# Kernel optimization log

Hardware: AMD Instinct MI355X
Metric: run time of the kernel (lower is better)

Reference implementation:

```python
import jax, jax.numpy as jnp
import numpy as np

BN_EPS = 1e-5
C = 128  # channels (hardcoded by feed_forward convs)


def _bn(v, gamma, beta, mean, var):
    # BatchNorm1d in inference form over channel axis of [B, C, N]
    scale = gamma / jnp.sqrt(var + BN_EPS)
    return (v - mean[:, None]) * scale[:, None] + beta[:, None]


def setup_inputs() -> dict:
    key = jax.random.key(0)
    ks = jax.random.split(key, 8)
    B, N = 8, 2048
    s = 0.05
    return {
        "x": jax.random.normal(ks[0], (B, N, C), jnp.float32),
        "Wq": jax.random.normal(ks[1], (C // 4, C), jnp.float32) * s,
        "Wk": jax.random.normal(ks[2], (C // 4, C), jnp.float32) * s,
        "Wv": jax.random.normal(ks[3], (C, C), jnp.float32) * s,
        "bv": jnp.zeros((C,), jnp.float32),
        "Wt": jax.random.normal(ks[4], (C, C), jnp.float32) * s,
        "bt": jnp.zeros((C,), jnp.float32),
        "g1": jnp.ones((C,), jnp.float32),
        "b1": jnp.zeros((C,), jnp.float32),
        "m1": jnp.zeros((C,), jnp.float32),
        "v1": jnp.ones((C,), jnp.float32),
        "W1": jax.random.normal(ks[5], (512, C), jnp.float32) * s,
        "bf1": jnp.zeros((512,), jnp.float32),
        "W2": jax.random.normal(ks[6], (C, 512), jnp.float32) * s,
        "bf2": jnp.zeros((C,), jnp.float32),
        "g2": jnp.ones((C,), jnp.float32),
        "b2": jnp.zeros((C,), jnp.float32),
        "m2": jnp.zeros((C,), jnp.float32),
        "v2": jnp.ones((C,), jnp.float32),
    }


def reference(x, Wq, Wk, Wv, bv, Wt, bt, g1, b1, m1, v1,
              W1, bf1, W2, bf2, g2, b2, m2, v2):
    # x: [B, N, C] -> work in [B, C, N] layout like the torch module
    xc = jnp.transpose(x, (0, 2, 1))                      # [B, C, N]
    # q_conv(x).permute -> [B, N, C/4]; k_conv -> [B, C/4, N]
    x_q = jnp.einsum('bnc,oc->bno', x, Wq)                # [B, N, C/4]
    x_k = jnp.einsum('bnc,oc->bon', x, Wk)                # [B, C/4, N]
    x_v = jnp.einsum('bnc,oc->bon', x, Wv) + bv[:, None]  # [B, C, N]

    energy = jnp.einsum('bnd,bdm->bnm', x_q, x_k)         # [B, N, N]
    scale = jnp.sqrt(jnp.asarray(C, x.dtype))             # sqrt(x_v.shape[-2])
    attention = jax.nn.softmax(energy / scale, axis=-1)   # [B, N, N]
    x_r = jnp.einsum('bcn,bnm->bcm', x_v, attention)      # [B, C, N]

    t = jnp.einsum('oc,bcn->bon', Wt, xc - x_r) + bt[:, None]
    x_r2 = jax.nn.relu(_bn(t, g1, b1, m1, v1))
    h = xc + x_r2                                         # [B, C, N]

    residual = h
    f = jax.nn.relu(jnp.einsum('oc,bcn->bon', W1, h) + bf1[:, None])
    f = jnp.einsum('of,bfn->bon', W2, f) + bf2[:, None]
    out = _bn(residual + f, g2, b2, m2, v2)               # [B, C, N]
    return jnp.transpose(out, (0, 2, 1))                  # [B, N, C]
```

## Files before the change

kernel.cpp:

```cpp
#include <hip/hip_runtime.h>
#include <hip/hip_bf16.h>

#define BDIM 256
#define NPTS (8 * 2048)
#define CC 128
#define DD 32
#define FF 512
#define NN 2048
#define SCALE 0.08838834764831845f

typedef float f32x4 __attribute__((ext_vector_type(4)));
typedef short s16x8 __attribute__((ext_vector_type(8)));
typedef unsigned short ushort_t;

__device__ __forceinline__ ushort_t bf16r(float x) {
    __hip_bfloat16 h = __float2bfloat16(x);
    return *reinterpret_cast<ushort_t*>(&h);
}
__device__ __forceinline__ float bf16tof(ushort_t u) {
    unsigned v = ((unsigned)u) << 16;
    return *reinterpret_cast<float*>(&v);
}
__device__ __forceinline__ unsigned pack2(float a, float b) {
    return ((unsigned)bf16r(b) << 16) | (unsigned)bf16r(a);
}

__global__ void k_cvt_all(const float* __restrict__ W1, const float* __restrict__ W2,
                          const float* __restrict__ Wq, const float* __restrict__ Wk,
                          const float* __restrict__ Wv, const float* __restrict__ Wt,
                          ushort_t* __restrict__ dst) {
    int i = blockIdx.x * BDIM + threadIdx.x;
    const float* src; int off;
    if (i < 16384)      { src = W1; off = 0; }
    else if (i < 32768) { src = W2; off = 16384; }
    else if (i < 33792) { src = Wq; off = 32768; }
    else if (i < 34816) { src = Wk; off = 33792; }
    else if (i < 38912) { src = Wv; off = 34816; }
    else                { src = Wt; off = 38912; }
    float4 v = ((const float4*)src)[i - off];
    *(uint2*)(dst + (long)i * 4) = make_uint2(pack2(v.x, v.y), pack2(v.z, v.w));
}

__global__ __launch_bounds__(256) void k_proj(
        const float* __restrict__ x, const ushort_t* __restrict__ Wb,
        const float* __restrict__ bv,
        ushort_t* __restrict__ qg, ushort_t* __restrict__ kg,
        ushort_t* __restrict__ vTg) {
    __shared__ ushort_t xs[32][136];
    __shared__ ushort_t qks[32][72];
    __shared__ ushort_t vs[32][136];
    long base = (long)blockIdx.x * 32;
    int b = (int)(base >> 11);
    int n0 = (int)(base & (NN - 1));
    int t = threadIdx.x, w = t >> 6, l = t & 63, a = l & 15, g = l >> 4;
    {
        const float4* xg4 = (const float4*)(x + base * CC);
        #pragma unroll
        for (int rep = 0; rep < 4; ++rep) {
            int i = rep * BDIM + t;
            float4 v4 = xg4[i];
            int p = i >> 5, c4 = (i & 31) * 4;
            *(uint2*)&xs[p][c4] = make_uint2(pack2(v4.x, v4.y), pack2(v4.z, v4.w));
        }
    }
    s16x8 bF[3][4];
    #pragma unroll
    for (int ct = 0; ct < 3; ++ct) {
        int ctg = w * 3 + ct;
        #pragma unroll
        for (int ki = 0; ki < 4; ++ki)
            bF[ct][ki] = *(const s16x8*)(Wb + ((long)(ctg * 16 + a)) * CC + ki * 32 + g * 8);
    }
    __syncthreads();
    #pragma unroll
    for (int rt = 0; rt < 2; ++rt) {
        s16x8 aF[4];
        #pragma unroll
        for (int ki = 0; ki < 4; ++ki)
            aF[ki] = *(const s16x8*)&xs[rt * 16 + a][ki * 32 + g * 8];
        #pragma unroll
        for (int ct = 0; ct < 3; ++ct) {
            f32x4 acc = (f32x4){0.f, 0.f, 0.f, 0.f};
            #pragma unroll
            for (int ki = 0; ki < 4; ++ki)
                acc = __builtin_amdgcn_mfma_f32_16x16x32_bf16(aF[ki], bF[ct][ki], acc, 0, 0, 0);
            int ctg = w * 3 + ct;
            int oc = ctg * 16 + a;
            float bias = (oc >= 64) ? bv[oc - 64] : 0.f;
            #pragma unroll
            for (int r = 0; r < 4; ++r) {
                int p = rt * 16 + g * 4 + r;
                float val = acc[r] + bias;
                if (oc < 64) qks[p][oc] = bf16r(val);
                else         vs[p][oc - 64] = bf16r(val);
            }
        }
    }
    __syncthreads();
    {
        int p = t >> 3, c = (t & 7) * 4;
        *(uint2*)(qg + (base + p) * DD + c) = *(const uint2*)&qks[p][c];
        *(uint2*)(kg + (base + p) * DD + c) = *(const uint2*)&qks[p][32 + c];
    }
    #pragma unroll
    for (int rep = 0; rep < 2; ++rep) {
        int i = rep * BDIM + t;
        int c = i & 127, nch = i >> 7;
        int p0 = nch * 8;
        uint4 r;
        r.x = (unsigned)vs[p0+0][c] | ((unsigned)vs[p0+1][c] << 16);
        r.y = (unsigned)vs[p0+2][c] | ((unsigned)vs[p0+3][c] << 16);
        r.z = (unsigned)vs[p0+4][c] | ((unsigned)vs[p0+5][c] << 16);
        r.w = (unsigned)vs[p0+6][c] | ((unsigned)vs[p0+7][c] << 16);
        *(uint4*)(vTg + ((long)(b * CC + c)) * NN + n0 + p0) = r;
    }
}

__global__ __launch_bounds__(256) void k_rowstats(
        const ushort_t* __restrict__ qg, const ushort_t* __restrict__ kg,
        float* __restrict__ rowinv) {
    __shared__ float ps[4][64];
    int b = blockIdx.x >> 5;
    int nt = (blockIdx.x & 31) * 64;
    int t = threadIdx.x, w = t >> 6, l = t & 63, a = l & 15, g = l >> 4;
    s16x8 qA[4];
    #pragma unroll
    for (int s = 0; s < 4; ++s)
        qA[s] = *(const s16x8*)(qg + ((long)(b * NN + nt + s*16 + a)) * DD + g*8);
    float sm[16];
    #pragma unroll
    for (int i = 0; i < 16; ++i) sm[i] = 0.f;
    s16x8 kB = *(const s16x8*)(kg + ((long)(b * NN + w * 16 + a)) * DD + g*8);
    for (int it = 0; it < 32; ++it) {
        s16x8 kBn;
        if (it < 31)
            kBn = *(const s16x8*)(kg + ((long)(b * NN + ((it+1)*4 + w)*16 + a)) * DD + g*8);
        #pragma unroll
        for (int s = 0; s < 4; ++s) {
            f32x4 D = (f32x4){0.f, 0.f, 0.f, 0.f};
            D = __builtin_amdgcn_mfma_f32_16x16x32_bf16(qA[s], kB, D, 0, 0, 0);
            #pragma unroll
            for (int r = 0; r < 4; ++r)
                sm[s * 4 + r] += __expf(D[r] * SCALE);
        }
        kB = kBn;
    }
    #pragma unroll
    for (int off = 1; off < 16; off <<= 1)
        #pragma unroll
        for (int ix = 0; ix < 16; ++ix)
            sm[ix] += __shfl_xor(sm[ix], off, 64);
    if (a == 0) {
        #pragma unroll
        for (int s = 0; s < 4; ++s)
            #pragma unroll
            for (int r = 0; r < 4; ++r)
                ps[w][s * 16 + g * 4 + r] = sm[s * 4 + r];
    }
    __syncthreads();
    if (t < 64) {
        float S = ps[0][t] + ps[1][t] + ps[2][t] + ps[3][t];
        rowinv[(long)b * NN + nt + t] = 1.f / S;
    }
}

__global__ __launch_bounds__(512) void k_pv(
        const ushort_t* __restrict__ qg, const ushort_t* __restrict__ kg,
        const ushort_t* __restrict__ vTg, const float* __restrict__ rowinv,
        const float* __restrict__ x, const ushort_t* __restrict__ Wtb,
        const float* __restrict__ bt,
        const float* __restrict__ g1, const float* __restrict__ b1,
        const float* __restrict__ m1, const float* __restrict__ v1,
        ushort_t* __restrict__ hb) {
    __shared__ ushort_t qs[2][64][40];
    __shared__ ushort_t ks[32][40];
    __shared__ ushort_t vTs[2][128][72];
    __shared__ ushort_t pT[32][72];
    __shared__ float rin_s[2][64];
    __shared__ ushort_t xb[32][136];
    __shared__ ushort_t ds[32][136];
    int b = blockIdx.x >> 6;
    int m0 = (blockIdx.x & 63) * 32;
    int t = threadIdx.x, w = t >> 6, l = t & 63, a = l & 15, g = l >> 4;
    int nsub = w & 3, msub = w >> 2;
    const ushort_t* vTb = vTg + (long)b * CC * NN;
    if (t < 128) {
        int r = t >> 2, o = (t & 3) * 8;
        *(s16x8*)&ks[r][o] = *(const s16x8*)(kg + ((long)(b * NN + m0 + r)) * DD + o);
    }
    int qr = t >> 2, qo = (t & 3) * 8;
    int c0 = t >> 3, vo0 = (t & 7) * 8;
    int c1 = (512 + t) >> 3, vo1 = (t & 7) * 8;
    uint4 qreg = make_uint4(0, 0, 0, 0), vreg0, vreg1;
    float rinreg = 0.f;
    if (t < 256) qreg = *(const uint4*)(qg + ((long)(b * NN + qr)) * DD + qo);
    vreg0 = *(const uint4*)(vTb + (long)c0 * NN + vo0);
    vreg1 = *(const uint4*)(vTb + (long)c1 * NN + vo1);
    if (t < 64) rinreg = rowinv[(long)b * NN + t];
    if (t < 256) *(uint4*)&qs[0][qr][qo] = qreg;
    *(uint4*)&vTs[0][c0][vo0] = vreg0;
    *(uint4*)&vTs[0][c1][vo1] = vreg1;
    if (t < 64) rin_s[0][t] = rinreg;

    f32x4 acc[2];
    acc[0] = (f32x4){0.f, 0.f, 0.f, 0.f};
    acc[1] = (f32x4){0.f, 0.f, 0.f, 0.f};
    int cur = 0;
    for (int it = 0; it < 32; ++it) {
        __syncthreads();
        int ntn = (it + 1) * 64;
        if (it < 31) {
            if (t < 256) qreg = *(const uint4*)(qg + ((long)(b * NN + ntn + qr)) * DD + qo);
            vreg0 = *(const uint4*)(vTb + (long)c0 * NN + ntn + vo0);
            vreg1 = *(const uint4*)(vTb + (long)c1 * NN + ntn + vo1);
            if (t < 64) rinreg = rowinv[(long)b * NN + ntn + t];
        }
        s16x8 qf = *(const s16x8*)&qs[cur][nsub * 16 + a][g * 8];
        s16x8 kf = *(const s16x8*)&ks[msub * 16 + a][g * 8];
        f32x4 e = (f32x4){0.f, 0.f, 0.f, 0.f};
        e = __builtin_amdgcn_mfma_f32_16x16x32_bf16(qf, kf, e, 0, 0, 0);
        float p[4];
        #pragma unroll
        for (int r = 0; r < 4; ++r)
            p[r] = __expf(e[r] * SCALE) * rin_s[cur][nsub * 16 + g * 4 + r];
        *(uint2*)&pT[msub * 16 + a][nsub * 16 + g * 4] =
            make_uint2(pack2(p[0], p[1]), pack2(p[2], p[3]));
        __syncthreads();
        #pragma unroll
        for (int k2 = 0; k2 < 2; ++k2) {
            s16x8 A0 = *(const s16x8*)&pT[a][k2 * 32 + g * 8];
            s16x8 A1 = *(const s16x8*)&pT[16 + a][k2 * 32 + g * 8];
            s16x8 Bf = *(const s16x8*)&vTs[cur][w * 16 + a][k2 * 32 + g * 8];
            acc[0] = __builtin_amdgcn_mfma_f32_16x16x32_bf16(A0, Bf, acc[0], 0, 0, 0);
            acc[1] = __builtin_amdgcn_mfma_f32_16x16x32_bf16(A1, Bf, acc[1], 0, 0, 0);
        }
        if (it < 31) {
            if (t < 256) *(uint4*)&qs[cur ^ 1][qr][qo] = qreg;
            *(uint4*)&vTs[cur ^ 1][c0][vo0] = vreg0;
            *(uint4*)&vTs[cur ^ 1][c1][vo1] = vreg1;
            if (t < 64) rin_s[cur ^ 1][t] = rinreg;
        }
        cur ^= 1;
    }
    long pbase = (long)b * NN + m0;
    {
        const float4* xg4 = (const float4*)(x + pbase * CC);
        #pragma unroll
        for (int rep = 0; rep < 2; ++rep) {
            int i = rep * 512 + t;
            float4 xv = xg4[i];
            int p = i >> 5, c4 = (i & 31) * 4;
            *(uint2*)&xb[p][c4] = make_uint2(pack2(xv.x, xv.y), pack2(xv.z, xv.w));
        }
    }
    __syncthreads();
    #pragma unroll
    for (int ms = 0; ms < 2; ++ms)
        #pragma unroll
        for (int r = 0; r < 4; ++r) {
            int ml = ms * 16 + g * 4 + r;
            int c = w * 16 + a;
            ds[ml][c] = bf16r(bf16tof(xb[ml][c]) - acc[ms][r]);
        }
    __syncthreads();
    {
        int ph = w & 1, fh = w >> 1;
        s16x8 aF[4];
        #pragma unroll
        for (int ki = 0; ki < 4; ++ki)
            aF[ki] = *(const s16x8*)&ds[ph * 16 + a][ki * 32 + g * 8];
        #pragma unroll
        for (int oi = 0; oi < 2; ++oi) {
            int ot = fh * 2 + oi;
            f32x4 ac = (f32x4){0.f, 0.f, 0.f, 0.f};
            #pragma unroll
            for (int ki = 0; ki < 4; ++ki) {
                s16x8 bF = *(const s16x8*)(Wtb + ((long)(ot * 16 + a)) * CC + ki * 32 + g * 8);
                ac = __builtin_amdgcn_mfma_f32_16x16x32_bf16(aF[ki], bF, ac, 0, 0, 0);
            }
            int o = ot * 16 + a;
            float sc = g1[o] * rsqrtf(v1[o] + 1e-5f);
            float mm = m1[o], bb = b1[o], bo = bt[o];
            #pragma unroll
            for (int r = 0; r < 4; ++r) {
                int p = ph * 16 + g * 4 + r;
                float tv = ((ac[r] + bo) - mm) * sc + bb;
                tv = fmaxf(tv, 0.f);
                hb[(pbase + p) * CC + o] = bf16r(bf16tof(xb[p][o]) + tv);
            }
        }
    }
}

__global__ __launch_bounds__(256) void k_ff(
        const ushort_t* __restrict__ hb, const ushort_t* __restrict__ W1b,
        const ushort_t* __restrict__ W2b,
        const float* __restrict__ bf1, const float* __restrict__ bf2,
        const float* __restrict__ g2, const float* __restrict__ b2,
        const float* __restrict__ m2, const float* __restrict__ v2,
        float* __restrict__ out) {
    __shared__ ushort_t hs[32][136];
    __shared__ ushort_t w1s[2][64][128];
    __shared__ ushort_t w2s[2][128][64];
    __shared__ ushort_t fss[32][72];
    long pbase = (long)blockIdx.x * 32;
    int t = threadIdx.x;
    int l = t & 63, wid = t >> 6;
    int ph = wid & 1, fh = wid >> 1;
    int lr = l & 15, lg = l >> 4;
    for (int i = t; i < 512; i += BDIM) {
        int r = i >> 4, c0 = (i & 15) * 8;
        *(uint4*)&hs[r][c0] = *(const uint4*)(hb + (pbase + r) * CC + c0);
    }
    #pragma unroll
    for (int rep = 0; rep < 4; ++rep) {
        int i = rep * BDIM + t;
        int r = i >> 4, c0 = (i & 15) * 8;
        *(uint4*)&w1s[0][r][c0 ^ ((r & 7) * 8)] = *(const uint4*)(W1b + (long)r * CC + c0);
    }
    #pragma unroll
    for (int rep = 0; rep < 4; ++rep) {
        int i = rep * BDIM + t;
        int r = i >> 3, c0 = (i & 7) * 8;
        *(uint4*)&w2s[0][r][c0 ^ ((r & 7) * 8)] = *(const uint4*)(W2b + (long)r * FF + c0);
    }
    __syncthreads();
    s16x8 hA[4];
    #pragma unroll
    for (int ki = 0; ki < 4; ++ki)
        hA[ki] = *(const s16x8*)&hs[ph * 16 + lr][ki * 32 + lg * 8];
    f32x4 acc2[4];
    #pragma unroll
    for (int i = 0; i < 4; ++i) acc2[i] = (f32x4){0.f, 0.f, 0.f, 0.f};

    int cur = 0;
    uint4 wrg0, wrg1, wrg2, wrg3, wrg4, wrg5, wrg6, wrg7;
    for (int fc = 0; fc < 8; ++fc) {
        if (fc) __syncthreads();
        int f0 = fc * 64;
        if (fc < 7) {
            int f0n = f0 + 64;
            int r1 = t >> 4, c1 = (t & 15) * 8;
            int r2 = t >> 3, c2 = (t & 7) * 8;
            wrg0 = *(const uint4*)(W1b + (long)(f0n + r1) * CC + c1);
            wrg1 = *(const uint4*)(W1b + (long)(f0n + 16 + r1) * CC + c1);
            wrg2 = *(const uint4*)(W1b + (long)(f0n + 32 + r1) * CC + c1);
            wrg3 = *(const uint4*)(W1b + (long)(f0n + 48 + r1) * CC + c1);
            wrg4 = *(const uint4*)(W2b + (long)r2 * FF + f0n + c2);
            wrg5 = *(const uint4*)(W2b + (long)(32 + r2) * FF + f0n + c2);
            wrg6 = *(const uint4*)(W2b + (long)(64 + r2) * FF + f0n + c2);
            wrg7 = *(const uint4*)(W2b + (long)(96 + r2) * FF + f0n + c2);
        }
        #pragma unroll
        for (int fi = 0; fi < 2; ++fi) {
            int ft = fh * 2 + fi;
            int row = ft * 16 + lr;
            f32x4 a1 = (f32x4){0.f, 0.f, 0.f, 0.f};
            #pragma unroll
            for (int ki = 0; ki < 4; ++ki) {
                int col = ki * 32 + lg * 8;
                s16x8 bfr = *(const s16x8*)&w1s[cur][row][col ^ ((row & 7) * 8)];
                a1 = __builtin_amdgcn_mfma_f32_16x16x32_bf16(hA[ki], bfr, a1, 0, 0, 0);
            }
            float bias = bf1[f0 + ft * 16 + lr];
            #pragma unroll
            for (int r = 0; r < 4; ++r) {
                float vv = fmaxf(a1[r] + bias, 0.f);
                fss[ph * 16 + lg * 4 + r][ft * 16 + lr] = bf16r(vv);
            }
        }
        __syncthreads();
        #pragma unroll
        for (int k2 = 0; k2 < 2; ++k2) {
            s16x8 afr = *(const s16x8*)&fss[ph * 16 + lr][k2 * 32 + lg * 8];
            #pragma unroll
            for (int oi = 0; oi < 4; ++oi) {
                int ot = fh * 4 + oi;
                int row = ot * 16 + lr;
                int col = k2 * 32 + lg * 8;
                s16x8 bfr = *(const s16x8*)&w2s[cur][row][col ^ ((row & 7) * 8)];
                acc2[oi] = __builtin_amdgcn_mfma_f32_16x16x32_bf16(afr, bfr, acc2[oi], 0, 0, 0);
            }
        }
        if (fc < 7) {
            int nb = cur ^ 1;
            int r1 = t >> 4, c1 = (t & 15) * 8;
            int r2 = t >> 3, c2 = (t & 7) * 8;
            *(uint4*)&w1s[nb][r1][c1 ^ ((r1 & 7) * 8)] = wrg0;
            *(uint4*)&w1s[nb][16 + r1][c1 ^ ((r1 & 7) * 8)] = wrg1;
            *(uint4*)&w1s[nb][32 + r1][c1 ^ ((r1 & 7) * 8)] = wrg2;
            *(uint4*)&w1s[nb][48 + r1][c1 ^ ((r1 & 7) * 8)] = wrg3;
            *(uint4*)&w2s[nb][r2][c2 ^ ((r2 & 7) * 8)] = wrg4;
            *(uint4*)&w2s[nb][32 + r2][c2 ^ (((32 + r2) & 7) * 8)] = wrg5;
            *(uint4*)&w2s[nb][64 + r2][c2 ^ (((64 + r2) & 7) * 8)] = wrg6;
            *(uint4*)&w2s[nb][96 + r2][c2 ^ (((96 + r2) & 7) * 8)] = wrg7;
            cur = nb;
        }
    }
    #pragma unroll
    for (int oi = 0; oi < 4; ++oi) {
        int o = (fh * 4 + oi) * 16 + lr;
        float sc = g2[o] * rsqrtf(v2[o] + 1e-5f);
        float mm = m2[o], bb = b2[o], bias2 = bf2[o];
        #pragma unroll
        for (int r = 0; r < 4; ++r) {
            int p = ph * 16 + lg * 4 + r;
            float val = bf16tof(hs[p][o]) + acc2[oi][r] + bias2;
            out[(pbase + p) * CC + o] = (val - mm) * sc + bb;
        }
    }
}

extern "C" void kernel_launch(void* const* d_in, const int* in_sizes, int n_in,
                              void* d_out, int out_size, void* d_ws, size_t ws_size,
                              hipStream_t stream) {
    const float* x   = (const float*)d_in[0];
    const float* Wq  = (const float*)d_in[1];
    const float* Wk  = (const float*)d_in[2];
    const float* Wv  = (const float*)d_in[3];
    const float* bv  = (const float*)d_in[4];
    const float* Wt  = (const float*)d_in[5];
    const float* bt  = (const float*)d_in[6];
    const float* g1  = (const float*)d_in[7];
    const float* b1  = (const float*)d_in[8];
    const float* m1  = (const float*)d_in[9];
    const float* v1  = (const float*)d_in[10];
    const float* W1  = (const float*)d_in[11];
    const float* bf1 = (const float*)d_in[12];
    const float* W2  = (const float*)d_in[13];
    const float* bf2 = (const float*)d_in[14];
    const float* g2  = (const float*)d_in[15];
    const float* b2  = (const float*)d_in[16];
    const float* m2  = (const float*)d_in[17];
    const float* v2  = (const float*)d_in[18];
    float* out = (float*)d_out;

    float* ws  = (float*)d_ws;
    float* rin = ws;
    ushort_t* qg   = (ushort_t*)(rin + NPTS);
    ushort_t* kg   = qg + (long)NPTS * DD;
    ushort_t* vTg  = kg + (long)NPTS * DD;
    ushort_t* hbuf = vTg + (long)NPTS * CC;
    ushort_t* W1b  = hbuf + (long)NPTS * CC;
    ushort_t* W2b  = W1b + FF * CC;
    ushort_t* Wb   = W2b + FF * CC;
    ushort_t* Wtb  = Wb + 192 * CC;

    k_cvt_all<<<168, BDIM, 0, stream>>>(W1, W2, Wq, Wk, Wv, Wt, W1b);
    k_proj<<<NPTS / 32, BDIM, 0, stream>>>(x, Wb, bv, qg, kg, vTg);
    k_rowstats<<<8 * (NN / 64), BDIM, 0, stream>>>(qg, kg, rin);
    k_pv<<<8 * (NN / 32), 512, 0, stream>>>(qg, kg, vTg, rin,
                                            x, Wtb, bt, g1, b1, m1, v1, hbuf);
    k_ff<<<NPTS / 32, BDIM, 0, stream>>>(hbuf, W1b, W2b, bf1, bf2, g2, b2, m2, v2, out);
}
```

Before: 80.62 us.

## Software-pipeline P·V loop with double-buffered P and triple-buffered V tiles

Restructures the k_pv attention loop so the QK/exp stage of tile it overlaps the P·V MFMA stage of tile it-1. P is double-buffered and V is triple-buffered, which removes one of the two block barriers per iteration. Shared memory is merged into a single arena that the epilogue buffers reuse after the loop, to offset the larger buffers. The cost is more LDS per block (about 76 KB), which may lower occupancy.

Measured after the change: 78.83 us. 1.02x faster.

```diff
diff --git a/kernel.cpp b/kernel.cpp
--- a/kernel.cpp
+++ b/kernel.cpp
@@ -172,13 +172,12 @@
         const float* __restrict__ g1, const float* __restrict__ b1,
         const float* __restrict__ m1, const float* __restrict__ v1,
         ushort_t* __restrict__ hb) {
-    __shared__ ushort_t qs[2][64][40];
-    __shared__ ushort_t ks[32][40];
-    __shared__ ushort_t vTs[2][128][72];
-    __shared__ ushort_t pT[32][72];
-    __shared__ float rin_s[2][64];
-    __shared__ ushort_t xb[32][136];
-    __shared__ ushort_t ds[32][136];
+    __shared__ __align__(16) char arena[77824];
+    auto vTs   = (ushort_t (*)[128][72])(arena);
+    auto qs    = (ushort_t (*)[64][40])(arena + 55296);
+    auto ks    = (ushort_t (*)[40])(arena + 65536);
+    auto pT    = (ushort_t (*)[32][72])(arena + 68096);
+    auto rin_s = (float (*)[64])(arena + 77312);
     int b = blockIdx.x >> 6;
     int m0 = (blockIdx.x & 63) * 32;
     int t = threadIdx.x, w = t >> 6, l = t & 63, a = l & 15, g = l >> 4;
@@ -201,47 +200,55 @@
     *(uint4*)&vTs[0][c0][vo0] = vreg0;
     *(uint4*)&vTs[0][c1][vo1] = vreg1;
     if (t < 64) rin_s[0][t] = rinreg;
-
     f32x4 acc[2];
     acc[0] = (f32x4){0.f, 0.f, 0.f, 0.f};
     acc[1] = (f32x4){0.f, 0.f, 0.f, 0.f};
-    int cur = 0;
-    for (int it = 0; it < 32; ++it) {
-        __syncthreads();
-        int ntn = (it + 1) * 64;
+    __syncthreads();
+    for (int it = 0; it <= 32; ++it) {
         if (it < 31) {
+            int ntn = (it + 1) * 64;
             if (t < 256) qreg = *(const uint4*)(qg + ((long)(b * NN + ntn + qr)) * DD + qo);
             vreg0 = *(const uint4*)(vTb + (long)c0 * NN + ntn + vo0);
             vreg1 = *(const uint4*)(vTb + (long)c1 * NN + ntn + vo1);
             if (t < 64) rinreg = rowinv[(long)b * NN + ntn + t];
         }
-        s16x8 qf = *(const s16x8*)&qs[cur][nsub * 16 + a][g * 8];
-        s16x8 kf = *(const s16x8*)&ks[msub * 16 + a][g * 8];
-        f32x4 e = (f32x4){0.f, 0.f, 0.f, 0.f};
-        e = __builtin_amdgcn_mfma_f32_16x16x32_bf16(qf, kf, e, 0, 0, 0);
-        float p[4];
-        #pragma unroll
-        for (int r = 0; r < 4; ++r)
-            p[r] = __expf(e[r] * SCALE) * rin_s[cur][nsub * 16 + g * 4 + r];
-        *(uint2*)&pT[msub * 16 + a][nsub * 16 + g * 4] =
-            make_uint2(pack2(p[0], p[1]), pack2(p[2], p[3]));
+        if (it < 32) {
+            int bq = it & 1;
+            s16x8 qf = *(const s16x8*)&qs[bq][nsub * 16 + a][g * 8];
+            s16x8 kf = *(const s16x8*)&ks[msub * 16 + a][g * 8];
+            f32x4 e = (f32x4){0.f, 0.f, 0.f, 0.f};
+            e = __builtin_amdgcn_mfma_f32_16x16x32_bf16(qf, kf, e, 0, 0, 0);
+            float p[4];
+            #pragma unroll
+            for (int r = 0; r < 4; ++r)
+                p[r] = __expf(e[r] * SCALE) * rin_s[bq][nsub * 16 + g * 4 + r];
+            *(uint2*)&pT[bq][msub * 16 + a][nsub * 16 + g * 4] =
+                make_uint2(pack2(p[0], p[1]), pack2(p[2], p[3]));
+        }
+        if (it >= 1) {
+            int pb = (it - 1) & 1;
+            int vb = (it - 1) % 3;
+            #pragma unroll
+            for (int k2 = 0; k2 < 2; ++k2) {
+                s16x8 A0 = *(const s16x8*)&pT[pb][a][k2 * 32 + g * 8];
+                s16x8 A1 = *(const s16x8*)&pT[pb][16 + a][k2 * 32 + g * 8];
+                s16x8 Bf = *(const s16x8*)&vTs[vb][w * 16 + a][k2 * 32 + g * 8];
+                acc[0] = __builtin_amdgcn_mfma_f32_16x16x32_bf16(A0, Bf, acc[0], 0, 0, 0);
+                acc[1] = __builtin_amdgcn_mfma_f32_16x16x32_bf16(A1, Bf, acc[1], 0, 0, 0);
+            }
+        }
+        if (it < 31) {
+            int bn = (it + 1) & 1;
+            int vn = (it + 1) % 3;
+            if (t < 256) *(uint4*)&qs[bn][qr][qo] = qreg;
+            *(uint4*)&vTs[vn][c0][vo0] = vreg0;
+            *(uint4*)&vTs[vn][c1][vo1] = vreg1;
+            if (t < 64) rin_s[bn][t] = rinreg;
+        }
         __syncthreads();
-        #pragma unroll
-        for (int k2 = 0; k2 < 2; ++k2) {
-            s16x8 A0 = *(const s16x8*)&pT[a][k2 * 32 + g * 8];
-            s16x8 A1 = *(const s16x8*)&pT[16 + a][k2 * 32 + g * 8];
-            s16x8 Bf = *(const s16x8*)&vTs[cur][w * 16 + a][k2 * 32 + g * 8];
-            acc[0] = __builtin_amdgcn_mfma_f32_16x16x32_bf16(A0, Bf, acc[0], 0, 0, 0);
-            acc[1] = __builtin_amdgcn_mfma_f32_16x16x32_bf16(A1, Bf, acc[1], 0, 0, 0);
-        }
-        if (it < 31) {
-            if (t < 256) *(uint4*)&qs[cur ^ 1][qr][qo] = qreg;
-            *(uint4*)&vTs[cur ^ 1][c0][vo0] = vreg0;
-            *(uint4*)&vTs[cur ^ 1][c1][vo1] = vreg1;
-            if (t < 64) rin_s[cur ^ 1][t] = rinreg;
-        }
-        cur ^= 1;
-    }
+    }
+    auto xb  = (ushort_t (*)[136])(arena);
+    auto dsx = (ushort_t (*)[136])(arena + 8704);
     long pbase = (long)b * NN + m0;
     {
         const float4* xg4 = (const float4*)(x + pbase * CC);
@@ -260,7 +267,7 @@
         for (int r = 0; r < 4; ++r) {
             int ml = ms * 16 + g * 4 + r;
             int c = w * 16 + a;
-            ds[ml][c] = bf16r(bf16tof(xb[ml][c]) - acc[ms][r]);
+            dsx[ml][c] = bf16r(bf16tof(xb[ml][c]) - acc[ms][r]);
         }
     __syncthreads();
     {
@@ -268,7 +275,7 @@
         s16x8 aF[4];
         #pragma unroll
         for (int ki = 0; ki < 4; ++ki)
-            aF[ki] = *(const s16x8*)&ds[ph * 16 + a][ki * 32 + g * 8];
+            aF[ki] = *(const s16x8*)&dsx[ph * 16 + a][ki * 32 + g * 8];
         #pragma unroll
         for (int oi = 0; oi < 2; ++oi) {
             int ot = fh * 2 + oi;
```
